# Kernel tuning notes

Hardware: AMD Instinct MI355X
Metric: run time of the kernel (lower is better)

Reference implementation:

```python
import jax, jax.numpy as jnp
import numpy as np

N = 50000      # nodes
E = 1_600_000  # edges (before self-loops)
G = 100        # graphs in batch
IN = 16        # in_channels
H1, C1 = 4, 32 # gat1 heads, per-head channels
H2, C2 = 1, 32 # gat2 heads, per-head channels
NEG_SLOPE = 0.2


def setup_inputs() -> dict:
    key = jax.random.key(0)
    ks = jax.random.split(key, 16)
    s = 0.1
    return {
        "x": jax.random.normal(ks[0], (N, IN), jnp.float32),
        "edge_index": jax.random.randint(ks[1], (2, E), 0, N, dtype=jnp.int64),
        "batch": jnp.sort(jax.random.randint(ks[2], (N,), 0, G, dtype=jnp.int64)),
        # GATConv 1: lin (no bias), att_src/att_dst, output bias (concat -> H1*C1)
        "W1": jax.random.normal(ks[3], (IN, H1 * C1), jnp.float32) * s,
        "att_src1": jax.random.normal(ks[4], (H1, C1), jnp.float32) * s,
        "att_dst1": jax.random.normal(ks[5], (H1, C1), jnp.float32) * s,
        "b1": jnp.zeros((H1 * C1,), jnp.float32),
        # GATConv 2
        "W2": jax.random.normal(ks[6], (H1 * C1, H2 * C2), jnp.float32) * s,
        "att_src2": jax.random.normal(ks[7], (H2, C2), jnp.float32) * s,
        "att_dst2": jax.random.normal(ks[8], (H2, C2), jnp.float32) * s,
        "b2": jnp.zeros((H2 * C2,), jnp.float32),
        # MLP head: Linear(32,64) -> ReLU -> Linear(64,1)
        "Wh1": jax.random.normal(ks[9], (C2, 64), jnp.float32) * s,
        "bh1": jnp.zeros((64,), jnp.float32),
        "Wh2": jax.random.normal(ks[10], (64, 1), jnp.float32) * s,
        "bh2": jnp.zeros((1,), jnp.float32),
    }


def gat_conv(x, src, dst, W, a_src, a_dst, bias, heads, ch):
    """PyG GATConv (self-loops already included in src/dst), eval mode."""
    n = x.shape[0]
    h = (x @ W).reshape(n, heads, ch)                 # [N,H,C]
    # per-node attention logits, then gather per edge
    a_s = jnp.einsum('nhc,hc->nh', h, a_src)          # [N,H]
    a_d = jnp.einsum('nhc,hc->nh', h, a_dst)
    e = jax.nn.leaky_relu(a_s[src] + a_d[dst], NEG_SLOPE)  # [E,H]
    # segment softmax over incoming edges of each destination node
    m = jax.ops.segment_max(e, dst, num_segments=n)   # [N,H]
    ex = jnp.exp(e - m[dst])
    denom = jax.ops.segment_sum(ex, dst, num_segments=n)
    alpha = ex / (denom[dst] + 1e-16)                 # [E,H]
    # weighted scatter-aggregate of source features
    out = jax.ops.segment_sum(alpha[:, :, None] * h[src], dst, num_segments=n)
    return out.reshape(n, heads * ch) + bias


def reference(x, edge_index, batch, W1, att_src1, att_dst1, b1,
              W2, att_src2, att_dst2, b2, Wh1, bh1, Wh2, bh2):
    n = x.shape[0]
    loops = jnp.arange(n, dtype=edge_index.dtype)
    src = jnp.concatenate([edge_index[0], loops])
    dst = jnp.concatenate([edge_index[1], loops])

    h = jax.nn.elu(gat_conv(x, src, dst, W1, att_src1, att_dst1, b1, H1, C1))
    h = jax.nn.elu(gat_conv(h, src, dst, W2, att_src2, att_dst2, b2, H2, C2))

    # global mean pool by graph id
    sums = jax.ops.segment_sum(h, batch, num_segments=G)          # [G,C2]
    cnts = jax.ops.segment_sum(jnp.ones((n,), h.dtype), batch, num_segments=G)
    pooled = sums / jnp.maximum(cnts, 1.0)[:, None]

    out = jax.nn.relu(pooled @ Wh1 + bh1) @ Wh2 + bh2             # [G,1]
    return out
```

## Files before the change

kernel.cpp:

```cpp
#include <hip/hip_runtime.h>
#include <hip/hip_fp16.h>
#include <math.h>

#define IN_CH 16
#define HC1 128
#define NH1 4
#define C2 32
#define HID 64
#define NEG 0.2f
#define CAP 10240
#define CHUNK 4096

__device__ __forceinline__ float lrelu_exp_fast(float z) {
    float lr = fmaxf(z, NEG * z);
    return __expf(lr);
}
__device__ __forceinline__ float elu_fast(float v) {
    return v > 0.f ? v : __expf(v) - 1.0f;
}

__device__ __forceinline__ void fma_mix_lo(float& acc, int hpack, float w) {
    asm("v_fma_mix_f32 %0, %1, %2, %0 op_sel:[0,0,0] op_sel_hi:[1,0,0]"
        : "+v"(acc) : "v"(hpack), "v"(w));
}
__device__ __forceinline__ void fma_mix_hi(float& acc, int hpack, float w) {
    asm("v_fma_mix_f32 %0, %1, %2, %0 op_sel:[1,0,0] op_sel_hi:[1,0,0]"
        : "+v"(acc) : "v"(hpack), "v"(w));
}

__global__ void k_front(const int* __restrict__ ei, int E, int N, int nchunk,
                        int* __restrict__ cursors, int* __restrict__ buckets,
                        const float* __restrict__ x, const float2* __restrict__ W1v,
                        const float2* __restrict__ att_s2, const float2* __restrict__ att_d2,
                        __half2* __restrict__ h1h, float* __restrict__ as1, float* __restrict__ ad1) {
    int bid = blockIdx.x;
    if (bid < nchunk) {
        __shared__ int cnt[256];
        __shared__ int base[256];
        __shared__ int pos[256];
        int t = threadIdx.x;
        int c0 = bid * CHUNK;
        int M = E + N;
        cnt[t] = 0;
        pos[t] = 0;
        __syncthreads();
        int srcv[16], dstv[16];
#pragma unroll
        for (int k = 0; k < 16; ++k) {
            int i = c0 + k * 256 + t;
            int s = -1, d = -1;
            if (i < M) {
                if (i < E) { s = ei[i]; d = ei[E + i]; }
                else       { s = d = i - E; }
                atomicAdd(&cnt[d >> 8], 1);
            }
            srcv[k] = s; dstv[k] = d;
        }
        __syncthreads();
        if (cnt[t] > 0) base[t] = atomicAdd(&cursors[t], cnt[t]);
        __syncthreads();
#pragma unroll
        for (int k = 0; k < 16; ++k) {
            int d = dstv[k];
            if (d >= 0) {
                int b = d >> 8;
                int p = base[b] + atomicAdd(&pos[b], 1);
                buckets[b * CAP + p] = (srcv[k] << 8) | (d & 255);
            }
        }
    } else {
        int wave = threadIdx.x >> 6;
        int lane = threadIdx.x & 63;
        int n = (bid - nchunk) * 4 + wave;
        if (n >= N) return;
        float xv = x[n * IN_CH + (lane & 15)];
        float ax = 0.f, ay = 0.f;
#pragma unroll
        for (int k = 0; k < IN_CH; ++k) {
            float xk = __shfl(xv, k, 16);
            float2 w = W1v[k * 64 + lane];
            ax += xk * w.x;
            ay += xk * w.y;
        }
        h1h[(size_t)n * 64 + lane] = __floats2half2_rn(ax, ay);
        float2 s2 = att_s2[lane], d2 = att_d2[lane];
        float vs = ax * s2.x + ay * s2.y;
        float vd = ax * d2.x + ay * d2.y;
#pragma unroll
        for (int o = 1; o < 16; o <<= 1) {
            vs += __shfl_xor(vs, o, 64);
            vd += __shfl_xor(vd, o, 64);
        }
        if ((lane & 15) == 0) {
            as1[n * NH1 + (lane >> 4)] = vs;
            ad1[n * NH1 + (lane >> 4)] = vd;
        }
    }
}

__global__ void k_build(const int* __restrict__ buckets, const int* __restrict__ cursors,
                        int N, int M,
                        int* __restrict__ offsets, int* __restrict__ elist) {
    __shared__ int sc[256];
    __shared__ int deg[256];
    __shared__ int cur[256];
    int b = blockIdx.x, t = threadIdx.x;
    int cv = cursors[t];
    sc[t] = cv;
    __syncthreads();
    for (int o = 1; o < 256; o <<= 1) {
        int a = (t >= o) ? sc[t - o] : 0;
        __syncthreads();
        sc[t] += a;
        __syncthreads();
    }
    int cnt = cursors[b];
    int gbase = sc[b] - cnt;
    int n0 = b << 8;
    const int* bk = buckets + b * CAP;
    deg[t] = 0;
    if (b == 0 && t == 0) offsets[N] = M;
    __syncthreads();
    for (int i = t; i < cnt; i += 256) atomicAdd(&deg[bk[i] & 255], 1);
    __syncthreads();
    int v = deg[t];
    sc[t] = v;
    __syncthreads();
    for (int o = 1; o < 256; o <<= 1) {
        int a = (t >= o) ? sc[t - o] : 0;
        __syncthreads();
        sc[t] += a;
        __syncthreads();
    }
    int excl = sc[t] - v;
    cur[t] = excl;
    if (n0 + t < N) offsets[n0 + t] = gbase + excl;
    __syncthreads();
    for (int i = t; i < cnt; i += 256) {
        int e = bk[i];
        int p = atomicAdd(&cur[e & 255], 1);
        elist[gbase + p] = e >> 8;
    }
}

__global__ void k_agg1(const int* __restrict__ offsets, const int* __restrict__ elist,
                       const char* __restrict__ as1b, const float* __restrict__ ad1,
                       const char* __restrict__ h1b, const float* __restrict__ b1,
                       const float* __restrict__ W2,
                       const float* __restrict__ aS2v, const float* __restrict__ aD2v,
                       int N, __half2* __restrict__ h2h,
                       float* __restrict__ as2, float* __restrict__ ad2) {
    __shared__ float swl[HC1][36];
    __shared__ float sxrow[4][HC1];
    int t = threadIdx.x;
    for (int i = t; i < HC1 * C2; i += 256)
        swl[i >> 5][i & 31] = W2[i];
    __syncthreads();

    int wave = t >> 6;
    int lane = t & 63;
    int n = blockIdx.x * 4 + wave;
    if (n >= N) return;

    int slot = lane >> 4, chunk = lane & 15, head = chunk >> 2;
    int lo = offsets[n], hi = offsets[n + 1];
    float adh = ad1[n * NH1 + head];
    unsigned coff = (unsigned)(chunk << 4);
    unsigned hoff = (unsigned)(head << 2);
    float acc[8];
#pragma unroll
    for (int j = 0; j < 8; ++j) acc[j] = 0.f;
    float sumw = 0.f;
    for (int e0 = lo; e0 < hi; e0 += 16) {
        unsigned s[4]; bool ok[4]; float z[4]; float4 v[4]; float w[4];
#pragma unroll
        for (int u = 0; u < 4; ++u) {
            int ee = e0 + 4 * u + slot;
            ok[u] = ee < hi;
            s[u] = (unsigned)elist[ok[u] ? ee : lo];
        }
#pragma unroll
        for (int u = 0; u < 4; ++u) {
            z[u] = *(const float*)(as1b + (s[u] * 16u + hoff));
            v[u] = *(const float4*)(h1b + (s[u] * 256u + coff));
        }
#pragma unroll
        for (int u = 0; u < 4; ++u)
            w[u] = ok[u] ? lrelu_exp_fast(z[u] + adh) : 0.f;
#pragma unroll
        for (int u = 0; u < 4; ++u) {
            const int* hp = (const int*)&v[u];
            fma_mix_lo(acc[0], hp[0], w[u]); fma_mix_hi(acc[1], hp[0], w[u]);
            fma_mix_lo(acc[2], hp[1], w[u]); fma_mix_hi(acc[3], hp[1], w[u]);
            fma_mix_lo(acc[4], hp[2], w[u]); fma_mix_hi(acc[5], hp[2], w[u]);
            fma_mix_lo(acc[6], hp[3], w[u]); fma_mix_hi(acc[7], hp[3], w[u]);
            sumw += w[u];
        }
    }
#pragma unroll
    for (int j = 0; j < 8; ++j) {
        acc[j] += __shfl_xor(acc[j], 16, 64);
        acc[j] += __shfl_xor(acc[j], 32, 64);
    }
    sumw += __shfl_xor(sumw, 16, 64);
    sumw += __shfl_xor(sumw, 32, 64);
    if (slot == 0) {
        float inv = 1.f / (sumw + 1e-16f);
        float4 ba = ((const float4*)b1)[2 * chunk];
        float4 bb = ((const float4*)b1)[2 * chunk + 1];
        float4 oa, ob;
        oa.x = elu_fast(acc[0] * inv + ba.x); oa.y = elu_fast(acc[1] * inv + ba.y);
        oa.z = elu_fast(acc[2] * inv + ba.z); oa.w = elu_fast(acc[3] * inv + ba.w);
        ob.x = elu_fast(acc[4] * inv + bb.x); ob.y = elu_fast(acc[5] * inv + bb.y);
        ob.z = elu_fast(acc[6] * inv + bb.z); ob.w = elu_fast(acc[7] * inv + bb.w);
        float4* dst4 = (float4*)&sxrow[wave][chunk * 8];
        dst4[0] = oa;
        dst4[1] = ob;
    }
    __builtin_amdgcn_wave_barrier();

    int c4 = (lane & 7) * 4;
    int kh = lane >> 3;
    float g0 = 0.f, g1 = 0.f, g2 = 0.f, g3 = 0.f;
    const float* xr = &sxrow[wave][kh * 16];
#pragma unroll
    for (int kk4 = 0; kk4 < 4; ++kk4) {
        float4 xv = *(const float4*)(xr + kk4 * 4);
#pragma unroll
        for (int j = 0; j < 4; ++j) {
            float x1 = (j == 0) ? xv.x : (j == 1) ? xv.y : (j == 2) ? xv.z : xv.w;
            float4 wv = *(const float4*)&swl[kh * 16 + kk4 * 4 + j][c4];
            g0 += x1 * wv.x; g1 += x1 * wv.y; g2 += x1 * wv.z; g3 += x1 * wv.w;
        }
    }
    g0 += __shfl_xor(g0, 8, 64); g0 += __shfl_xor(g0, 16, 64); g0 += __shfl_xor(g0, 32, 64);
    g1 += __shfl_xor(g1, 8, 64); g1 += __shfl_xor(g1, 16, 64); g1 += __shfl_xor(g1, 32, 64);
    g2 += __shfl_xor(g2, 8, 64); g2 += __shfl_xor(g2, 16, 64); g2 += __shfl_xor(g2, 32, 64);
    g3 += __shfl_xor(g3, 8, 64); g3 += __shfl_xor(g3, 16, 64); g3 += __shfl_xor(g3, 32, 64);
    if (lane < 8) {
        h2h[(size_t)n * 16 + (c4 >> 1)]     = __floats2half2_rn(g0, g1);
        h2h[(size_t)n * 16 + (c4 >> 1) + 1] = __floats2half2_rn(g2, g3);
        float ps = g0 * aS2v[c4] + g1 * aS2v[c4 + 1] + g2 * aS2v[c4 + 2] + g3 * aS2v[c4 + 3];
        float pd = g0 * aD2v[c4] + g1 * aD2v[c4 + 1] + g2 * aD2v[c4 + 2] + g3 * aD2v[c4 + 3];
        ps += __shfl_xor(ps, 1, 64); ps += __shfl_xor(ps, 2, 64); ps += __shfl_xor(ps, 4, 64);
        pd += __shfl_xor(pd, 1, 64); pd += __shfl_xor(pd, 2, 64); pd += __shfl_xor(pd, 4, 64);
        if (lane == 0) { as2[n] = ps; ad2[n] = pd; }
    }
}

__global__ void k_agg2(const int* __restrict__ offsets, const int* __restrict__ elist,
                       const char* __restrict__ as2b, const float* __restrict__ ad2,
                       const char* __restrict__ h2b, const float* __restrict__ b2,
                       int N, float* __restrict__ out2) {
    int wave = threadIdx.x >> 6;
    int lane = threadIdx.x & 63;
    int n = blockIdx.x * 4 + wave;
    if (n >= N) return;
    int slot = lane >> 2, chunk = lane & 3;
    int lo = offsets[n], hi = offsets[n + 1];
    float ad = ad2[n];
    unsigned coff = (unsigned)(chunk << 4);
    float acc[8];
#pragma unroll
    for (int j = 0; j < 8; ++j) acc[j] = 0.f;
    float sumw = 0.f;
    for (int e0 = lo; e0 < hi; e0 += 32) {
        unsigned s[2]; bool ok[2]; float z[2]; float4 v[2]; float w[2];
#pragma unroll
        for (int u = 0; u < 2; ++u) {
            int ee = e0 + 16 * u + slot;
            ok[u] = ee < hi;
            s[u] = (unsigned)elist[ok[u] ? ee : lo];
        }
#pragma unroll
        for (int u = 0; u < 2; ++u) {
            z[u] = *(const float*)(as2b + (s[u] * 4u));
            v[u] = *(const float4*)(h2b + (s[u] * 64u + coff));
        }
#pragma unroll
        for (int u = 0; u < 2; ++u)
            w[u] = ok[u] ? lrelu_exp_fast(z[u] + ad) : 0.f;
#pragma unroll
        for (int u = 0; u < 2; ++u) {
            const int* hp = (const int*)&v[u];
            fma_mix_lo(acc[0], hp[0], w[u]); fma_mix_hi(acc[1], hp[0], w[u]);
            fma_mix_lo(acc[2], hp[1], w[u]); fma_mix_hi(acc[3], hp[1], w[u]);
            fma_mix_lo(acc[4], hp[2], w[u]); fma_mix_hi(acc[5], hp[2], w[u]);
            fma_mix_lo(acc[6], hp[3], w[u]); fma_mix_hi(acc[7], hp[3], w[u]);
            sumw += w[u];
        }
    }
#pragma unroll
    for (int j = 0; j < 8; ++j) {
        acc[j] += __shfl_xor(acc[j], 4, 64);
        acc[j] += __shfl_xor(acc[j], 8, 64);
        acc[j] += __shfl_xor(acc[j], 16, 64);
        acc[j] += __shfl_xor(acc[j], 32, 64);
    }
    sumw += __shfl_xor(sumw, 4, 64);
    sumw += __shfl_xor(sumw, 8, 64);
    sumw += __shfl_xor(sumw, 16, 64);
    sumw += __shfl_xor(sumw, 32, 64);
    if (slot == 0) {
        float inv = 1.f / (sumw + 1e-16f);
        float4 ba = ((const float4*)b2)[2 * chunk];
        float4 bb = ((const float4*)b2)[2 * chunk + 1];
        float o[8];
        o[0] = elu_fast(acc[0] * inv + ba.x); o[1] = elu_fast(acc[1] * inv + ba.y);
        o[2] = elu_fast(acc[2] * inv + ba.z); o[3] = elu_fast(acc[3] * inv + ba.w);
        o[4] = elu_fast(acc[4] * inv + bb.x); o[5] = elu_fast(acc[5] * inv + bb.y);
        o[6] = elu_fast(acc[6] * inv + bb.z); o[7] = elu_fast(acc[7] * inv + bb.w);
        float* dst = out2 + (size_t)n * C2 + 8 * chunk;
        *(float4*)dst = make_float4(o[0], o[1], o[2], o[3]);
        *(float4*)(dst + 4) = make_float4(o[4], o[5], o[6], o[7]);
    }
}

__global__ void k_pool(const float* __restrict__ out2, const int* __restrict__ batch,
                       int N, const float* __restrict__ Wh1, const float* __restrict__ bh1,
                       const float* __restrict__ Wh2, const float* __restrict__ bh2,
                       float* __restrict__ out) {
    int g = blockIdx.x;
    int t = threadIdx.x;
    __shared__ int sb[2];
    __shared__ float pooled[C2];
    __shared__ float red[256];
    if (t < 2) {
        int target = g + t;
        int lo = 0, hi = N;
        while (lo < hi) { int mid = (lo + hi) >> 1; if (batch[mid] < target) lo = mid + 1; else hi = mid; }
        sb[t] = lo;
    }
    __syncthreads();
    int lo = sb[0], hi = sb[1];
    int c = t & 31, grp = t >> 5;
    float part = 0.f;
    for (int n = lo + grp; n < hi; n += 8) part += out2[n * C2 + c];
    red[t] = part;
    __syncthreads();
    if (t < 128) red[t] += red[t + 128];
    __syncthreads();
    if (t < 64) red[t] += red[t + 64];
    __syncthreads();
    if (t < 32) {
        red[t] += red[t + 32];
        float cnt = (float)(hi - lo);
        pooled[t] = red[t] / fmaxf(cnt, 1.f);
    }
    __syncthreads();
    float hval = 0.f;
    if (t < HID) {
        float a = bh1[t];
#pragma unroll
        for (int cc = 0; cc < C2; ++cc) a += pooled[cc] * Wh1[cc * HID + t];
        hval = fmaxf(a, 0.f) * Wh2[t];
    }
    if (t < 64) {
        for (int o = 32; o > 0; o >>= 1) hval += __shfl_down(hval, o, 64);
        if (t == 0) out[g] = hval + bh2[0];
    }
}

extern "C" void kernel_launch(void* const* d_in, const int* in_sizes, int n_in,
                              void* d_out, int out_size, void* d_ws, size_t ws_size,
                              hipStream_t stream) {
    const float* x    = (const float*)d_in[0];
    const int*   ei   = (const int*)d_in[1];
    const int*   batch= (const int*)d_in[2];
    const float* W1   = (const float*)d_in[3];
    const float* aS1  = (const float*)d_in[4];
    const float* aD1  = (const float*)d_in[5];
    const float* b1   = (const float*)d_in[6];
    const float* W2   = (const float*)d_in[7];
    const float* aS2  = (const float*)d_in[8];
    const float* aD2  = (const float*)d_in[9];
    const float* b2   = (const float*)d_in[10];
    const float* Wh1  = (const float*)d_in[11];
    const float* bh1  = (const float*)d_in[12];
    const float* Wh2  = (const float*)d_in[13];
    const float* bh2  = (const float*)d_in[14];
    float* out = (float*)d_out;

    int N = in_sizes[2];
    int E = in_sizes[1] / 2;
    int M = E + N;
    int G = out_size;
    int nbk = (N + 255) >> 8;
    int nchunk = (M + CHUNK - 1) / CHUNK;
    int nlin = (N + 3) / 4;

    char* p = (char*)d_ws;
    auto alloc = [&](size_t bytes) -> void* {
        void* r = (void*)p;
        p += (bytes + 255) & ~(size_t)255;
        return r;
    };
    __half2* h1h   = (__half2*)alloc((size_t)N * 64 * 4);
    __half2* h2h   = (__half2*)alloc((size_t)N * 16 * 4);
    float* as1     = (float*)alloc((size_t)N * NH1 * 4);
    float* ad1     = (float*)alloc((size_t)N * NH1 * 4);
    float* as2     = (float*)alloc((size_t)N * 4);
    float* ad2     = (float*)alloc((size_t)N * 4);
    float* out2    = (float*)alloc((size_t)N * C2 * 4);
    int*   offsets = (int*)alloc((size_t)(N + 1) * 4);
    int*   elist   = (int*)alloc((size_t)M * 4);
    int*   cursors = (int*)alloc(256 * 4);
    int*   buckets = (int*)alloc((size_t)nbk * CAP * 4);

    hipMemsetAsync(cursors, 0, 256 * 4, stream);
    k_front<<<nchunk + nlin, 256, 0, stream>>>(ei, E, N, nchunk, cursors, buckets,
                                               x, (const float2*)W1, (const float2*)aS1,
                                               (const float2*)aD1, h1h, as1, ad1);
    k_build<<<nbk, 256, 0, stream>>>(buckets, cursors, N, M, offsets, elist);
    k_agg1<<<(N + 3) / 4, 256, 0, stream>>>(offsets, elist, (const char*)as1, ad1,
                                            (const char*)h1h, b1, W2, aS2, aD2,
                                            N, h2h, as2, ad2);
    k_agg2<<<(N + 3) / 4, 256, 0, stream>>>(offsets, elist, (const char*)as2, ad2,
                                            (const char*)h2h, b2, N, out2);
    k_pool<<<G, 256, 0, stream>>>(out2, batch, N, Wh1, bh1, Wh2, bh2, out);
}
```

Before: 275.2 us.

## Split CSR build blocks per bucket half and swizzle W2 shared layout

k_build now launches two blocks per 256-node bucket. Each block handles one 128-node half, so it scans the bucket but only counts and scatters its own half's edges, doubling block-level parallelism for the CSR construction. Separately, k_agg1 stores W2 and the per-wave activation row in shared memory with XOR/rotation swizzles to avoid LDS bank conflicts in the small dense projection. The cost is that every bucket's edges are read twice and there is extra index arithmetic.

```diff
diff --git a/kernel.cpp b/kernel.cpp
--- a/kernel.cpp
+++ b/kernel.cpp
@@ -102,9 +102,10 @@
                         int N, int M,
                         int* __restrict__ offsets, int* __restrict__ elist) {
     __shared__ int sc[256];
-    __shared__ int deg[256];
-    __shared__ int cur[256];
-    int b = blockIdx.x, t = threadIdx.x;
+    __shared__ int deg[128];
+    __shared__ int cur[128];
+    int b = blockIdx.x >> 1, half = blockIdx.x & 1;
+    int t = threadIdx.x;
     int cv = cursors[t];
     sc[t] = cv;
     __syncthreads();
@@ -115,46 +116,64 @@
         __syncthreads();
     }
     int cnt = cursors[b];
-    int gbase = sc[b] - cnt;
-    int n0 = b << 8;
+    int gbase_bucket = sc[b] - cnt;
+    int n0 = (b << 8) + (half << 7);
     const int* bk = buckets + b * CAP;
-    deg[t] = 0;
-    if (b == 0 && t == 0) offsets[N] = M;
-    __syncthreads();
-    for (int i = t; i < cnt; i += 256) atomicAdd(&deg[bk[i] & 255], 1);
-    __syncthreads();
-    int v = deg[t];
-    sc[t] = v;
-    __syncthreads();
-    for (int o = 1; o < 256; o <<= 1) {
-        int a = (t >= o) ? sc[t - o] : 0;
-        __syncthreads();
-        sc[t] += a;
-        __syncthreads();
-    }
-    int excl = sc[t] - v;
-    cur[t] = excl;
-    if (n0 + t < N) offsets[n0 + t] = gbase + excl;
+    if (t < 128) deg[t] = 0;
+    if (blockIdx.x == 0 && t == 0) offsets[N] = M;
+    __syncthreads();
+    for (int i = t; i < cnt; i += 256) {
+        int dl = bk[i] & 255;
+        if ((dl >> 7) == half) atomicAdd(&deg[dl & 127], 1);
+    }
+    __syncthreads();
+    int v = (t < 128) ? deg[t] : 0;
+    if (t < 128) sc[t] = v;
+    __syncthreads();
+    for (int o = 1; o < 128; o <<= 1) {
+        int a = (t < 128 && t >= o) ? sc[t - o] : 0;
+        __syncthreads();
+        if (t < 128) sc[t] += a;
+        __syncthreads();
+    }
+    __shared__ int gbh;
+    if (t == 127) {
+        int S = sc[127];
+        gbh = (half == 0) ? gbase_bucket : gbase_bucket + (cnt - S);
+    }
+    __syncthreads();
+    int gbase = gbh;
+    if (t < 128) {
+        int excl = sc[t] - v;
+        cur[t] = excl;
+        if (n0 + t < N) offsets[n0 + t] = gbase + excl;
+    }
     __syncthreads();
     for (int i = t; i < cnt; i += 256) {
         int e = bk[i];
-        int p = atomicAdd(&cur[e & 255], 1);
-        elist[gbase + p] = e >> 8;
+        int dl = e & 255;
+        if ((dl >> 7) == half) {
+            int p = atomicAdd(&cur[dl & 127], 1);
+            elist[gbase + p] = e >> 8;
+        }
     }
 }
 
 __global__ void k_agg1(const int* __restrict__ offsets, const int* __restrict__ elist,
                        const char* __restrict__ as1b, const float* __restrict__ ad1,
                        const char* __restrict__ h1b, const float* __restrict__ b1,
-                       const float* __restrict__ W2,
+                       const float4* __restrict__ W2q,
                        const float* __restrict__ aS2v, const float* __restrict__ aD2v,
                        int N, __half2* __restrict__ h2h,
                        float* __restrict__ as2, float* __restrict__ ad2) {
-    __shared__ float swl[HC1][36];
-    __shared__ float sxrow[4][HC1];
+    __shared__ float4 swz[HC1 * 8];
+    __shared__ float4 sxr[4][32];
     int t = threadIdx.x;
-    for (int i = t; i < HC1 * C2; i += 256)
-        swl[i >> 5][i & 31] = W2[i];
+    for (int q = t; q < HC1 * 8; q += 256) {
+        int k = q >> 3, c4g = q & 7;
+        int phys = (q & ~7) | ((c4g + (k >> 4)) & 7);
+        swz[phys] = W2q[q];
+    }
     __syncthreads();
 
     int wave = t >> 6;
@@ -213,23 +232,24 @@
         oa.z = elu_fast(acc[2] * inv + ba.z); oa.w = elu_fast(acc[3] * inv + ba.w);
         ob.x = elu_fast(acc[4] * inv + bb.x); ob.y = elu_fast(acc[5] * inv + bb.y);
         ob.z = elu_fast(acc[6] * inv + bb.z); ob.w = elu_fast(acc[7] * inv + bb.w);
-        float4* dst4 = (float4*)&sxrow[wave][chunk * 8];
-        dst4[0] = oa;
-        dst4[1] = ob;
+        int q0 = chunk * 2, q1 = q0 + 1;
+        sxr[wave][q0 ^ (q0 >> 2)] = oa;
+        sxr[wave][q1 ^ (q1 >> 2)] = ob;
     }
     __builtin_amdgcn_wave_barrier();
 
-    int c4 = (lane & 7) * 4;
-    int kh = lane >> 3;
+    int c4g = lane & 7, kh = lane >> 3;
+    int c4 = c4g * 4;
     float g0 = 0.f, g1 = 0.f, g2 = 0.f, g3 = 0.f;
-    const float* xr = &sxrow[wave][kh * 16];
 #pragma unroll
     for (int kk4 = 0; kk4 < 4; ++kk4) {
-        float4 xv = *(const float4*)(xr + kk4 * 4);
+        int qx = kh * 4 + kk4;
+        float4 xv = sxr[wave][qx ^ (qx >> 2)];
 #pragma unroll
         for (int j = 0; j < 4; ++j) {
             float x1 = (j == 0) ? xv.x : (j == 1) ? xv.y : (j == 2) ? xv.z : xv.w;
-            float4 wv = *(const float4*)&swl[kh * 16 + kk4 * 4 + j][c4];
+            int k = kh * 16 + kk4 * 4 + j;
+            float4 wv = swz[(k << 3) | ((c4g + kh) & 7)];
             g0 += x1 * wv.x; g1 += x1 * wv.y; g2 += x1 * wv.z; g3 += x1 * wv.w;
         }
     }
@@ -411,10 +431,10 @@
     k_front<<<nchunk + nlin, 256, 0, stream>>>(ei, E, N, nchunk, cursors, buckets,
                                                x, (const float2*)W1, (const float2*)aS1,
                                                (const float2*)aD1, h1h, as1, ad1);
-    k_build<<<nbk, 256, 0, stream>>>(buckets, cursors, N, M, offsets, elist);
+    k_build<<<2 * nbk, 256, 0, stream>>>(buckets, cursors, N, M, offsets, elist);
     k_agg1<<<(N + 3) / 4, 256, 0, stream>>>(offsets, elist, (const char*)as1, ad1,
-                                            (const char*)h1h, b1, W2, aS2, aD2,
-                                            N, h2h, as2, ad2);
+                                            (const char*)h1h, b1, (const float4*)W2,
+                                            aS2, aD2, N, h2h, as2, ad2);
     k_agg2<<<(N + 3) / 4, 256, 0, stream>>>(offsets, elist, (const char*)as2, ad2,
                                             (const char*)h2h, b2, N, out2);
     k_pool<<<G, 256, 0, stream>>>(out2, batch, N, Wh1, bh1, Wh2, bh2, out);
```

After: 274.9 us. About the same (-0.1%).
